# Optimization experiments

Hardware: AMD Instinct MI355X
Metric: run time of the kernel (lower is better)

## Reference

```python
import jax, jax.numpy as jnp
import numpy as np

STATE = 24
ACT = 6
L1 = 100
L2 = 100
CHOL = ACT * (ACT + 1) // 2  # 21
BATCH = 262144


def setup_inputs() -> dict:
    key = jax.random.key(0)
    ks = jax.random.split(key, 9)
    return {
        "states": jax.random.normal(ks[0], (BATCH, STATE), jnp.float32),
        "W1": jax.random.normal(ks[1], (L1, STATE), jnp.float32) * (1.0 / np.sqrt(STATE)),
        "b1": jax.random.normal(ks[2], (L1,), jnp.float32) * 0.01,
        "W2": jax.random.normal(ks[3], (L2, L1), jnp.float32) * (1.0 / np.sqrt(L1)),
        "b2": jax.random.normal(ks[4], (L2,), jnp.float32) * 0.01,
        "Wm": jax.random.normal(ks[5], (ACT, L2), jnp.float32) * (1.0 / np.sqrt(L2)),
        "bm": jax.random.normal(ks[6], (ACT,), jnp.float32) * 0.01,
        "Wc": jax.random.normal(ks[7], (CHOL, L2), jnp.float32) * (1.0 / np.sqrt(L2)),
        "bc": jax.random.normal(ks[8], (CHOL,), jnp.float32) * 0.01,
    }


def reference(states, W1, b1, W2, b2, Wm, bm, Wc, bc):
    # 2-layer MLP backbone
    x = jax.nn.relu(states @ W1.T + b1)          # [B, L1]
    x = jax.nn.relu(x @ W2.T + b2)               # [B, L2]
    mean = jnp.tanh(x @ Wm.T + bm)               # [B, ACT]
    chol_vec = jax.nn.softplus(x @ Wc.T + bc)    # [B, CHOL]
    # Vectorized lower-triangular fill (replaces python double loop + .item()).
    # torch loop fills (i,j) with j<=i in row-major order == tril_indices order.
    rows, cols = jnp.tril_indices(ACT)
    chol = jnp.zeros((states.shape[0], ACT, ACT), chol_vec.dtype).at[:, rows, cols].set(chol_vec)
    return mean, chol
```

## Files before the change

kernel.cpp:

```cpp
#include <hip/hip_runtime.h>
#include <hip/hip_bf16.h>
#include <math.h>

typedef short bf16x8 __attribute__((ext_vector_type(8)));
typedef short bf16x4 __attribute__((ext_vector_type(4)));
typedef float f32x4 __attribute__((ext_vector_type(4)));

#define STATE 24
#define L1N 100

#define IMG_W2_U32 2000
#define IMG_U32 10752
#define W1_STRIDE 40
#define K_STRIDE 136

#define W2_HALVES 13600
#define WH_HALVES 3672
#define X_OFF (W2_HALVES + WH_HALVES)
#define X_HALVES (16 * K_STRIDE)
#define LDS_HALVES (X_OFF + 4 * X_HALVES)
#define LDS_BYTES (LDS_HALVES * 2)
#define GRID 768

__device__ __constant__ int CHOFF[21] = {0,6,7,12,13,14,18,19,20,21,24,25,26,27,28,30,31,32,33,34,35};
__device__ __constant__ int ZOFF[15]  = {1,2,3,4,5,8,9,10,11,15,16,17,22,23,29};

__device__ inline unsigned short f2bf(float f) {
    union { float f; unsigned u; } v; v.f = f;
    unsigned r = v.u + 0x7FFFu + ((v.u >> 16) & 1u);
    return (unsigned short)(r >> 16);
}
__device__ inline unsigned pkbf(float lo, float hi) {
    __hip_bfloat162 h = __float22bfloat162_rn(float2{lo, hi});
    return *(const unsigned*)&h;
}
__device__ inline float fast_tanh(float x) {
    float e = __builtin_amdgcn_exp2f(x * 2.8853900817779268f);
    return 1.0f - 2.0f * __builtin_amdgcn_rcpf(e + 1.0f);
}
__device__ inline float fast_softplus(float v) {
    float u = __builtin_amdgcn_exp2f(fabsf(v) * -1.4426950408889634f);
    float l = __builtin_amdgcn_logf(1.0f + u) * 0.6931471805599453f;
    return fmaxf(v, 0.0f) + l;
}

__global__ __launch_bounds__(256) void prep_weights(
    const float* __restrict__ W1, const float* __restrict__ b1,
    const float* __restrict__ W2, const float* __restrict__ b2,
    const float* __restrict__ Wm, const float* __restrict__ bm,
    const float* __restrict__ Wc, const float* __restrict__ bc,
    unsigned* __restrict__ img)
{
    int i = blockIdx.x * 256 + threadIdx.x;
    if (i >= IMG_U32) return;
    float lo = 0.f, hi = 0.f;
    if (i < 2000) {
        int r = i / 20, k = (i % 20) * 2;
        if (k < STATE)      { lo = W1[r * STATE + k]; hi = W1[r * STATE + k + 1]; }
        else if (k == STATE)  lo = b1[r];
    } else if (i < 8800) {
        int j = i - 2000, r = j / 68, k = (j % 68) * 2;
        if (k < L1N)      { lo = W2[r * L1N + k]; hi = (k + 1 < L1N) ? W2[r * L1N + k + 1] : 0.f; }
        else if (k == L1N)  lo = b2[r];
    } else if (i < 10636) {
        int j = i - 8800, r = j / 68, k = (j % 68) * 2;
        const float* src; float bias;
        if (r < 6) { src = Wm + r * L1N; bias = bm[r]; }
        else       { src = Wc + (r - 6) * L1N; bias = bc[r - 6]; }
        if (k < L1N)      { lo = src[k]; hi = (k + 1 < L1N) ? src[k + 1] : 0.f; }
        else if (k == L1N)  lo = bias;
    }
    img[i] = pkbf(lo, hi);
}

__global__ __launch_bounds__(256, 3) void actor_mfma(
    const float* __restrict__ states,
    const unsigned* __restrict__ img,
    float* __restrict__ out_mean, float* __restrict__ out_chol, int ntiles)
{
    extern __shared__ __align__(16) unsigned short smem[];
    const int tid = threadIdx.x;
    {
        const uint4* src = (const uint4*)(img + IMG_W2_U32);
        uint4* dst = (uint4*)smem;
        for (int i = tid; i < (IMG_U32 - IMG_W2_U32) / 4; i += 256) dst[i] = src[i];
    }
    const int wave = tid >> 6, lane = tid & 63, q = lane >> 4, c = lane & 15;
    unsigned short* W2s = smem;
    unsigned short* Whs = smem + W2_HALVES;
    unsigned short* X   = smem + X_OFF + wave * X_HALVES;
    unsigned* Xw  = (unsigned*)X;
    float* stage  = (float*)X;

    bf16x8 wf1[7];
    #pragma unroll
    for (int nt = 0; nt < 7; ++nt) {
        int wr = nt * 16 + c; wr = wr < L1N ? wr : L1N - 1;
        wf1[nt] = *(const bf16x8*)((const unsigned short*)img + wr * W1_STRIDE + q * 8);
    }

    __syncthreads();

    #pragma unroll
    for (int it = 0; it < 5; ++it) {
        int idx = it * 64 + lane;
        if (idx < 288) {
            int r = idx / 18, s = idx - r * 18;
            Xw[r * 68 + 50 + s] = (s == 0) ? 0x00003F80u : 0u;
        }
    }

    int scol[8], skind[8];
    #pragma unroll
    for (int ht = 0; ht < 2; ++ht)
        #pragma unroll
        for (int i = 0; i < 4; ++i) {
            int f = ht * 16 + q * 4 + i, e = ht * 4 + i;
            if (f < 6)       { scol[e] = 36 + f;        skind[e] = 0; }
            else if (f < 27) { scol[e] = CHOFF[f - 6];  skind[e] = 1; }
            else             { scol[e] = 0;             skind[e] = -1; }
        }
    int zcol[4];
    const int nz = (q == 3) ? 3 : 4;
    #pragma unroll
    for (int z = 0; z < 4; ++z) zcol[z] = ZOFF[(q * 4 + z) < 15 ? (q * 4 + z) : 14];

    float4 sv[2];
    auto loadStates = [&](int tt) {
        if (tt < ntiles && q < 3) {
            const float* p = states + ((long)tt * 64 + wave * 16 + c) * STATE + q * 8;
            sv[0] = *(const float4*)p;
            sv[1] = *(const float4*)(p + 4);
        }
    };
    loadStates(blockIdx.x);

    for (int t = blockIdx.x; t < ntiles; t += GRID) {
        const long rowW = (long)t * 64 + wave * 16;

        union { bf16x8 v; unsigned u[4]; } sb;
        if (q < 3) {
            sb.u[0] = pkbf(sv[0].x, sv[0].y); sb.u[1] = pkbf(sv[0].z, sv[0].w);
            sb.u[2] = pkbf(sv[1].x, sv[1].y); sb.u[3] = pkbf(sv[1].z, sv[1].w);
        } else {
            sb.u[0] = 0x00003F80u; sb.u[1] = sb.u[2] = sb.u[3] = 0u;
        }
        loadStates(t + GRID);

        #pragma unroll
        for (int nt = 0; nt < 7; ++nt) {
            f32x4 acc = {0.f, 0.f, 0.f, 0.f};
            acc = __builtin_amdgcn_mfma_f32_16x16x32_bf16(wf1[nt], sb.v, acc, 0, 0, 0);
            if (nt * 16 + q * 4 < L1N) {
                bf16x4 pk;
                #pragma unroll
                for (int i = 0; i < 4; ++i) pk[i] = (short)f2bf(fmaxf(acc[i], 0.f));
                *(bf16x4*)&X[c * K_STRIDE + nt * 16 + q * 4] = pk;
            }
        }

        bf16x8 ab[4];
        #pragma unroll
        for (int ks = 0; ks < 4; ++ks)
            ab[ks] = *(const bf16x8*)&X[c * K_STRIDE + ks * 32 + q * 8];
        f32x4 acc2[7];
        #pragma unroll
        for (int nt = 0; nt < 7; ++nt) acc2[nt] = (f32x4){0.f, 0.f, 0.f, 0.f};
        #pragma unroll
        for (int ks = 0; ks < 4; ++ks)
            #pragma unroll
            for (int nt = 0; nt < 7; ++nt) {
                int wr = nt * 16 + c; wr = wr < L1N ? wr : L1N - 1;
                bf16x8 wf = *(const bf16x8*)&W2s[wr * K_STRIDE + ks * 32 + q * 8];
                acc2[nt] = __builtin_amdgcn_mfma_f32_16x16x32_bf16(wf, ab[ks], acc2[nt], 0, 0, 0);
            }
        #pragma unroll
        for (int nt = 0; nt < 7; ++nt)
            if (nt * 16 + q * 4 < L1N) {
                bf16x4 pk;
                #pragma unroll
                for (int i = 0; i < 4; ++i) pk[i] = (short)f2bf(fmaxf(acc2[nt][i], 0.f));
                *(bf16x4*)&X[c * K_STRIDE + nt * 16 + q * 4] = pk;
            }

        bf16x8 ab3[4];
        #pragma unroll
        for (int ks = 0; ks < 4; ++ks)
            ab3[ks] = *(const bf16x8*)&X[c * K_STRIDE + ks * 32 + q * 8];
        f32x4 acc3[2];
        acc3[0] = (f32x4){0.f, 0.f, 0.f, 0.f};
        acc3[1] = (f32x4){0.f, 0.f, 0.f, 0.f};
        #pragma unroll
        for (int ks = 0; ks < 4; ++ks)
            #pragma unroll
            for (int ht = 0; ht < 2; ++ht) {
                int wr = ht * 16 + c; wr = wr < 27 ? wr : 26;
                bf16x8 wf = *(const bf16x8*)&Whs[wr * K_STRIDE + ks * 32 + q * 8];
                acc3[ht] = __builtin_amdgcn_mfma_f32_16x16x32_bf16(wf, ab3[ks], acc3[ht], 0, 0, 0);
            }

        #pragma unroll
        for (int e = 0; e < 8; ++e) {
            float v = acc3[e >> 2][e & 3];
            if (skind[e] == 0)      stage[c * 68 + scol[e]] = fast_tanh(v);
            else if (skind[e] == 1) stage[c * 68 + scol[e]] = fast_softplus(v);
        }
        #pragma unroll
        for (int z = 0; z < 4; ++z)
            if (z < nz) stage[c * 68 + zcol[z]] = 0.f;

        if (lane < 48) {
            float2 m = *(const float2*)&stage[(lane / 3) * 68 + 36 + (lane % 3) * 2];
            *(float2*)(out_mean + rowW * 6 + lane * 2) = m;
        }
        #pragma unroll
        for (int it = 0; it < 3; ++it) {
            int j = it * 64 + lane;
            if (j < 144) {
                float4 v = *(const float4*)&stage[(j / 9) * 68 + (j % 9) * 4];
                *(float4*)(out_chol + rowW * 36 + j * 4) = v;
            }
        }
    }
}

extern "C" void kernel_launch(void* const* d_in, const int* in_sizes, int n_in,
                              void* d_out, int out_size, void* d_ws, size_t ws_size,
                              hipStream_t stream) {
    const float* states = (const float*)d_in[0];
    const float* W1 = (const float*)d_in[1];
    const float* b1 = (const float*)d_in[2];
    const float* W2 = (const float*)d_in[3];
    const float* b2 = (const float*)d_in[4];
    const float* Wm = (const float*)d_in[5];
    const float* bm = (const float*)d_in[6];
    const float* Wc = (const float*)d_in[7];
    const float* bc = (const float*)d_in[8];

    const int batch = in_sizes[0] / STATE;
    float* out_mean = (float*)d_out;
    float* out_chol = out_mean + (size_t)batch * 6;
    unsigned* img = (unsigned*)d_ws;

    hipFuncSetAttribute((const void*)actor_mfma,
                        hipFuncAttributeMaxDynamicSharedMemorySize, LDS_BYTES);

    prep_weights<<<(IMG_U32 + 255) / 256, 256, 0, stream>>>(W1, b1, W2, b2,
                                                            Wm, bm, Wc, bc, img);
    const int ntiles = batch / 64;
    actor_mfma<<<GRID, 256, LDS_BYTES, stream>>>(states, img, out_mean, out_chol, ntiles);
}
```

Before: 113.2 us.

## Keep W2 and head weights in registers instead of LDS

Each wave now loads its W2 and head weight fragments from the workspace image straight into registers once, then reuses them for every tile. This removes the per-block LDS copy and the repeated LDS reads of weights inside the MFMA loops, and the layer-2 loop is reordered to accumulate one output tile at a time. The LDS allocation shrinks to the per-wave activation buffers only. In exchange, register pressure rises sharply, so launch bounds drop to 2 blocks per CU and the grid goes from 768 to 512 blocks, with a risk of lower occupancy or register spills.

```diff
diff --git a/kernel.cpp b/kernel.cpp
--- a/kernel.cpp
+++ b/kernel.cpp
@@ -9,18 +9,14 @@
 #define STATE 24
 #define L1N 100
 
-#define IMG_W2_U32 2000
 #define IMG_U32 10752
 #define W1_STRIDE 40
 #define K_STRIDE 136
-
-#define W2_HALVES 13600
-#define WH_HALVES 3672
-#define X_OFF (W2_HALVES + WH_HALVES)
+#define W2_HOFF 4000
+#define WH_HOFF 17600
+
 #define X_HALVES (16 * K_STRIDE)
-#define LDS_HALVES (X_OFF + 4 * X_HALVES)
-#define LDS_BYTES (LDS_HALVES * 2)
-#define GRID 768
+#define GRID 512
 
 __device__ __constant__ int CHOFF[21] = {0,6,7,12,13,14,18,19,20,21,24,25,26,27,28,30,31,32,33,34,35};
 __device__ __constant__ int ZOFF[15]  = {1,2,3,4,5,8,9,10,11,15,16,17,22,23,29};
@@ -73,39 +69,41 @@
     img[i] = pkbf(lo, hi);
 }
 
-__global__ __launch_bounds__(256, 3) void actor_mfma(
+__global__ __launch_bounds__(256, 2) void actor_mfma(
     const float* __restrict__ states,
     const unsigned* __restrict__ img,
     float* __restrict__ out_mean, float* __restrict__ out_chol, int ntiles)
 {
-    extern __shared__ __align__(16) unsigned short smem[];
+    __shared__ __align__(16) unsigned short smem[4 * X_HALVES];
     const int tid = threadIdx.x;
-    {
-        const uint4* src = (const uint4*)(img + IMG_W2_U32);
-        uint4* dst = (uint4*)smem;
-        for (int i = tid; i < (IMG_U32 - IMG_W2_U32) / 4; i += 256) dst[i] = src[i];
-    }
     const int wave = tid >> 6, lane = tid & 63, q = lane >> 4, c = lane & 15;
-    unsigned short* W2s = smem;
-    unsigned short* Whs = smem + W2_HALVES;
-    unsigned short* X   = smem + X_OFF + wave * X_HALVES;
-    unsigned* Xw  = (unsigned*)X;
-    float* stage  = (float*)X;
-
-    bf16x8 wf1[7];
+    unsigned short* X  = smem + wave * X_HALVES;
+    unsigned* Xw = (unsigned*)X;
+    float* stage = (float*)X;
+
+    const unsigned short* imgh = (const unsigned short*)img;
+    bf16x8 wf1[7], wf2[4][7], wf3[4][2];
     #pragma unroll
     for (int nt = 0; nt < 7; ++nt) {
         int wr = nt * 16 + c; wr = wr < L1N ? wr : L1N - 1;
-        wf1[nt] = *(const bf16x8*)((const unsigned short*)img + wr * W1_STRIDE + q * 8);
-    }
-
-    __syncthreads();
-
-    #pragma unroll
-    for (int it = 0; it < 5; ++it) {
+        wf1[nt] = *(const bf16x8*)(imgh + wr * W1_STRIDE + q * 8);
+        #pragma unroll
+        for (int ks = 0; ks < 4; ++ks)
+            wf2[ks][nt] = *(const bf16x8*)(imgh + W2_HOFF + wr * K_STRIDE + ks * 32 + q * 8);
+    }
+    #pragma unroll
+    for (int ht = 0; ht < 2; ++ht) {
+        int wr = ht * 16 + c; wr = wr < 27 ? wr : 26;
+        #pragma unroll
+        for (int ks = 0; ks < 4; ++ks)
+            wf3[ks][ht] = *(const bf16x8*)(imgh + WH_HOFF + wr * K_STRIDE + ks * 32 + q * 8);
+    }
+
+    #pragma unroll
+    for (int it = 0; it < 4; ++it) {
         int idx = it * 64 + lane;
-        if (idx < 288) {
-            int r = idx / 18, s = idx - r * 18;
+        if (idx < 224) {
+            int r = idx / 14, s = idx - r * 14;
             Xw[r * 68 + 50 + s] = (s == 0) ? 0x00003F80u : 0u;
         }
     }
@@ -163,25 +161,19 @@
         #pragma unroll
         for (int ks = 0; ks < 4; ++ks)
             ab[ks] = *(const bf16x8*)&X[c * K_STRIDE + ks * 32 + q * 8];
-        f32x4 acc2[7];
-        #pragma unroll
-        for (int nt = 0; nt < 7; ++nt) acc2[nt] = (f32x4){0.f, 0.f, 0.f, 0.f};
-        #pragma unroll
-        for (int ks = 0; ks < 4; ++ks)
+        #pragma unroll
+        for (int nt = 0; nt < 7; ++nt) {
+            f32x4 acc = {0.f, 0.f, 0.f, 0.f};
             #pragma unroll
-            for (int nt = 0; nt < 7; ++nt) {
-                int wr = nt * 16 + c; wr = wr < L1N ? wr : L1N - 1;
-                bf16x8 wf = *(const bf16x8*)&W2s[wr * K_STRIDE + ks * 32 + q * 8];
-                acc2[nt] = __builtin_amdgcn_mfma_f32_16x16x32_bf16(wf, ab[ks], acc2[nt], 0, 0, 0);
-            }
-        #pragma unroll
-        for (int nt = 0; nt < 7; ++nt)
+            for (int ks = 0; ks < 4; ++ks)
+                acc = __builtin_amdgcn_mfma_f32_16x16x32_bf16(wf2[ks][nt], ab[ks], acc, 0, 0, 0);
             if (nt * 16 + q * 4 < L1N) {
                 bf16x4 pk;
                 #pragma unroll
-                for (int i = 0; i < 4; ++i) pk[i] = (short)f2bf(fmaxf(acc2[nt][i], 0.f));
+                for (int i = 0; i < 4; ++i) pk[i] = (short)f2bf(fmaxf(acc[i], 0.f));
                 *(bf16x4*)&X[c * K_STRIDE + nt * 16 + q * 4] = pk;
             }
+        }
 
         bf16x8 ab3[4];
         #pragma unroll
@@ -193,11 +185,8 @@
         #pragma unroll
         for (int ks = 0; ks < 4; ++ks)
             #pragma unroll
-            for (int ht = 0; ht < 2; ++ht) {
-                int wr = ht * 16 + c; wr = wr < 27 ? wr : 26;
-                bf16x8 wf = *(const bf16x8*)&Whs[wr * K_STRIDE + ks * 32 + q * 8];
-                acc3[ht] = __builtin_amdgcn_mfma_f32_16x16x32_bf16(wf, ab3[ks], acc3[ht], 0, 0, 0);
-            }
+            for (int ht = 0; ht < 2; ++ht)
+                acc3[ht] = __builtin_amdgcn_mfma_f32_16x16x32_bf16(wf3[ks][ht], ab3[ks], acc3[ht], 0, 0, 0);
 
         #pragma unroll
         for (int e = 0; e < 8; ++e) {
@@ -242,11 +231,8 @@
     float* out_chol = out_mean + (size_t)batch * 6;
     unsigned* img = (unsigned*)d_ws;
 
-    hipFuncSetAttribute((const void*)actor_mfma,
-                        hipFuncAttributeMaxDynamicSharedMemorySize, LDS_BYTES);
-
     prep_weights<<<(IMG_U32 + 255) / 256, 256, 0, stream>>>(W1, b1, W2, b2,
                                                             Wm, bm, Wc, bc, img);
     const int ntiles = batch / 64;
-    actor_mfma<<<GRID, 256, LDS_BYTES, stream>>>(states, img, out_mean, out_chol, ntiles);
-}
+    actor_mfma<<<GRID, 256, 0, stream>>>(states, img, out_mean, out_chol, ntiles);
+}
```

New measurement: 114.0 us. About the same (+0.6%).
